# Performance work log

Hardware: AMD Instinct MI355X
Metric: run time of the kernel (lower is better)

Reference implementation:

```python
import jax, jax.numpy as jnp
import numpy as np

B, N_IN, N_MID, N_OUT = 262144, 64, 128, 32


def setup_inputs() -> dict:
    key = jax.random.key(0)
    kx, k1, kb1, k2, kb2 = jax.random.split(key, 5)
    v1 = 1.0 / np.sqrt(N_IN)   # per-synapse init range sqrt(1/len(dendrites))
    v2 = 1.0 / np.sqrt(N_MID)
    return {
        "x": jax.random.normal(kx, (B, N_IN), dtype=jnp.float32),
        "W1": jax.random.uniform(k1, (N_IN, N_MID), minval=-v1, maxval=v1, dtype=jnp.float32),
        "b1": jnp.zeros((N_MID,), dtype=jnp.float32),  # obtain_float_parameter inits biases to 0.0
        "W2": jax.random.uniform(k2, (N_MID, N_OUT), minval=-v2, maxval=v2, dtype=jnp.float32),
        "b2": jnp.zeros((N_OUT,), dtype=jnp.float32),
    }


def reference(x, W1, b1, W2, b2):
    # RegularNeuron: sum_i k_ij * x_i + b_j, then ReLU
    h = jax.nn.relu(x @ W1 + b1)          # [B, N_MID]
    # Output DestinationNeuron: sum_j k_jo * h_j + b_o, no activation
    y = h @ W2 + b2                        # [B, N_OUT]
    return y
```

## Files before the change

### kernel.cpp

```cpp
#include <hip/hip_runtime.h>
#include <hip/hip_bf16.h>

#define B_ROWS 262144
#define N_TILES (B_ROWS / 16)

typedef short short8 __attribute__((ext_vector_type(8)));
typedef float f32x4 __attribute__((ext_vector_type(4)));

__device__ inline short f2bf(float f) {
    __hip_bfloat16 h = __float2bfloat16(f);
    return __builtin_bit_cast(short, h);
}
__device__ inline unsigned pk2(float a, float b) {
    unsigned lo = (unsigned short)f2bf(a);
    unsigned hi = (unsigned short)f2bf(b);
    return lo | (hi << 16);
}

__global__ __launch_bounds__(256, 2) void livenet_mlp(
    const float* __restrict__ x, const float* __restrict__ W1,
    const float* __restrict__ b1, const float* __restrict__ W2,
    const float* __restrict__ b2, float* __restrict__ y) {
    __shared__ __align__(16) short hbuf[4 * 2048];

    const int tid  = threadIdx.x;
    const int wid  = tid >> 6;
    const int lane = tid & 63;
    const int g    = lane >> 4;
    const int q    = lane & 15;
    short* hb = hbuf + wid * 2048;
    const int key = 2 * (q & 7);

    short8 w1f[2][8];
#pragma unroll
    for (int ks = 0; ks < 2; ++ks)
#pragma unroll
        for (int n = 0; n < 8; ++n) {
            short8 v;
#pragma unroll
            for (int j = 0; j < 8; ++j)
                v[j] = f2bf(W1[(ks * 32 + g * 8 + j) * 128 + n * 16 + q]);
            w1f[ks][n] = v;
        }
    short8 w2f[4][2];
#pragma unroll
    for (int ks = 0; ks < 4; ++ks)
#pragma unroll
        for (int n = 0; n < 2; ++n) {
            short8 v;
#pragma unroll
            for (int j = 0; j < 8; ++j)
                v[j] = f2bf(W2[(ks * 32 + g * 8 + j) * 32 + n * 16 + q]);
            w2f[ks][n] = v;
        }
    f32x4 binit1[8], binit2[2];
#pragma unroll
    for (int n = 0; n < 8; ++n)
        binit1[n] = *(const f32x4*)(b1 + n * 16 + 4 * g);
#pragma unroll
    for (int n = 0; n < 2; ++n)
        binit2[n] = *(const f32x4*)(b2 + n * 16 + 4 * g);

    const int gwave = blockIdx.x * 4 + wid;
    const int S     = gridDim.x * 4;

    const float* xl = x + (size_t)q * 64 + g * 8;

    f32x4 c0, c1, c2, c3, m0, m1, m2, m3;
    {
        const f32x4* p = (const f32x4*)(xl + (size_t)gwave * 1024);
        c0 = p[0]; c1 = p[1]; c2 = p[8]; c3 = p[9];
    }
    {
        const f32x4* p = (const f32x4*)(xl + (size_t)(gwave + S) * 1024);
        m0 = p[0]; m1 = p[1]; m2 = p[8]; m3 = p[9];
    }

    for (int tile = gwave; tile < N_TILES; tile += S) {
        const int t2 = (tile + 2 * S < N_TILES) ? (tile + 2 * S) : tile;
        f32x4 p0, p1, p2, p3;
        {
            const f32x4* p = (const f32x4*)(xl + (size_t)t2 * 1024);
            p0 = p[0]; p1 = p[1]; p2 = p[8]; p3 = p[9];
        }

        const int row0 = tile * 16;

        short8 a0, a1;
        {
            short8 v;
            v[0] = f2bf(c0[0]); v[1] = f2bf(c0[1]); v[2] = f2bf(c0[2]); v[3] = f2bf(c0[3]);
            v[4] = f2bf(c1[0]); v[5] = f2bf(c1[1]); v[6] = f2bf(c1[2]); v[7] = f2bf(c1[3]);
            a0 = v;
            v[0] = f2bf(c2[0]); v[1] = f2bf(c2[1]); v[2] = f2bf(c2[2]); v[3] = f2bf(c2[3]);
            v[4] = f2bf(c3[0]); v[5] = f2bf(c3[1]); v[6] = f2bf(c3[2]); v[7] = f2bf(c3[3]);
            a1 = v;
        }

        f32x4 acc1[8];
#pragma unroll
        for (int n = 0; n < 8; ++n) {
            acc1[n] = __builtin_amdgcn_mfma_f32_16x16x32_bf16(w1f[0][n], a0, binit1[n], 0, 0, 0);
            acc1[n] = __builtin_amdgcn_mfma_f32_16x16x32_bf16(w1f[1][n], a1, acc1[n], 0, 0, 0);
        }

#pragma unroll
        for (int n = 0; n < 8; ++n) {
            float h0 = fmaxf(acc1[n][0], 0.0f);
            float h1 = fmaxf(acc1[n][1], 0.0f);
            float h2 = fmaxf(acc1[n][2], 0.0f);
            float h3 = fmaxf(acc1[n][3], 0.0f);
            uint2 w;
            w.x = pk2(h0, h1);
            w.y = pk2(h2, h3);
            const int cbp = (4 * n + g) ^ key;
            ((uint2*)hb)[q * 32 + cbp] = w;
        }

        short8 ha[4];
#pragma unroll
        for (int ks = 0; ks < 4; ++ks) {
            const int cbr = (8 * ks + 2 * g) ^ key;
            ha[ks] = *(const short8*)&hb[q * 128 + 4 * cbr];
        }

        f32x4 acc2[2];
#pragma unroll
        for (int n = 0; n < 2; ++n) {
            acc2[n] = __builtin_amdgcn_mfma_f32_16x16x32_bf16(w2f[0][n], ha[0], binit2[n], 0, 0, 0);
#pragma unroll
            for (int ks = 1; ks < 4; ++ks)
                acc2[n] = __builtin_amdgcn_mfma_f32_16x16x32_bf16(w2f[ks][n], ha[ks], acc2[n], 0, 0, 0);
        }

#pragma unroll
        for (int n = 0; n < 2; ++n)
            __builtin_nontemporal_store(
                acc2[n], (f32x4*)(y + (size_t)(row0 + q) * 32 + n * 16 + 4 * g));

        c0 = m0; c1 = m1; c2 = m2; c3 = m3;
        m0 = p0; m1 = p1; m2 = p2; m3 = p3;
    }
}

extern "C" void kernel_launch(void* const* d_in, const int* in_sizes, int n_in,
                              void* d_out, int out_size, void* d_ws, size_t ws_size,
                              hipStream_t stream) {
    const float* x  = (const float*)d_in[0];
    const float* W1 = (const float*)d_in[1];
    const float* b1 = (const float*)d_in[2];
    const float* W2 = (const float*)d_in[3];
    const float* b2 = (const float*)d_in[4];
    float* y = (float*)d_out;

    const int blocks = 512;
    livenet_mlp<<<blocks, 256, 0, stream>>>(x, W1, b1, W2, b2, y);
}
```

Baseline: 24.80 us.

## Stage weights through LDS with coalesced loads, shorten prefetch depth, plain stores

```diff
diff --git a/kernel.cpp b/kernel.cpp
--- a/kernel.cpp
+++ b/kernel.cpp
@@ -22,6 +22,9 @@
     const float* __restrict__ b1, const float* __restrict__ W2,
     const float* __restrict__ b2, float* __restrict__ y) {
     __shared__ __align__(16) short hbuf[4 * 2048];
+    __shared__ __align__(16) short w1t[128 * 64];
+    __shared__ __align__(16) short w2t[32 * 128];
+    __shared__ __align__(16) float bls[160];
 
     const int tid  = threadIdx.x;
     const int wid  = tid >> 6;
@@ -31,57 +34,60 @@
     short* hb = hbuf + wid * 2048;
     const int key = 2 * (q & 7);
 
+#pragma unroll
+    for (int p = 0; p < 8; ++p) {
+        const int idx = p * 1024 + tid * 4;
+        f32x4 v = *(const f32x4*)(W1 + idx);
+        const int k = idx >> 7, c = idx & 127;
+#pragma unroll
+        for (int e = 0; e < 4; ++e) w1t[(c + e) * 64 + k] = f2bf(v[e]);
+    }
+#pragma unroll
+    for (int p = 0; p < 4; ++p) {
+        const int idx = p * 1024 + tid * 4;
+        f32x4 v = *(const f32x4*)(W2 + idx);
+        const int k = idx >> 5, o = idx & 31;
+#pragma unroll
+        for (int e = 0; e < 4; ++e) w2t[(o + e) * 128 + k] = f2bf(v[e]);
+    }
+    if (tid < 128) bls[tid] = b1[tid];
+    else if (tid < 160) bls[tid] = b2[tid - 128];
+    __syncthreads();
+
     short8 w1f[2][8];
 #pragma unroll
     for (int ks = 0; ks < 2; ++ks)
 #pragma unroll
-        for (int n = 0; n < 8; ++n) {
-            short8 v;
-#pragma unroll
-            for (int j = 0; j < 8; ++j)
-                v[j] = f2bf(W1[(ks * 32 + g * 8 + j) * 128 + n * 16 + q]);
-            w1f[ks][n] = v;
-        }
+        for (int n = 0; n < 8; ++n)
+            w1f[ks][n] = *(const short8*)&w1t[(n * 16 + q) * 64 + ks * 32 + g * 8];
     short8 w2f[4][2];
 #pragma unroll
     for (int ks = 0; ks < 4; ++ks)
 #pragma unroll
-        for (int n = 0; n < 2; ++n) {
-            short8 v;
-#pragma unroll
-            for (int j = 0; j < 8; ++j)
-                v[j] = f2bf(W2[(ks * 32 + g * 8 + j) * 32 + n * 16 + q]);
-            w2f[ks][n] = v;
-        }
+        for (int n = 0; n < 2; ++n)
+            w2f[ks][n] = *(const short8*)&w2t[(n * 16 + q) * 128 + ks * 32 + g * 8];
     f32x4 binit1[8], binit2[2];
 #pragma unroll
-    for (int n = 0; n < 8; ++n)
-        binit1[n] = *(const f32x4*)(b1 + n * 16 + 4 * g);
+    for (int n = 0; n < 8; ++n) binit1[n] = *(const f32x4*)&bls[n * 16 + 4 * g];
 #pragma unroll
-    for (int n = 0; n < 2; ++n)
-        binit2[n] = *(const f32x4*)(b2 + n * 16 + 4 * g);
+    for (int n = 0; n < 2; ++n) binit2[n] = *(const f32x4*)&bls[128 + n * 16 + 4 * g];
 
     const int gwave = blockIdx.x * 4 + wid;
     const int S     = gridDim.x * 4;
-
     const float* xl = x + (size_t)q * 64 + g * 8;
 
-    f32x4 c0, c1, c2, c3, m0, m1, m2, m3;
+    f32x4 c0, c1, c2, c3;
     {
         const f32x4* p = (const f32x4*)(xl + (size_t)gwave * 1024);
         c0 = p[0]; c1 = p[1]; c2 = p[8]; c3 = p[9];
     }
-    {
-        const f32x4* p = (const f32x4*)(xl + (size_t)(gwave + S) * 1024);
-        m0 = p[0]; m1 = p[1]; m2 = p[8]; m3 = p[9];
-    }
 
     for (int tile = gwave; tile < N_TILES; tile += S) {
-        const int t2 = (tile + 2 * S < N_TILES) ? (tile + 2 * S) : tile;
+        const int tn = (tile + S < N_TILES) ? (tile + S) : tile;
         f32x4 p0, p1, p2, p3;
         {
-            const f32x4* p = (const f32x4*)(xl + (size_t)t2 * 1024);
-            p0 = p[0]; p1 = p[1]; p2 = p[8]; p3 = p[9];
+            const f32x4* pp = (const f32x4*)(xl + (size_t)tn * 1024);
+            p0 = pp[0]; p1 = pp[1]; p2 = pp[8]; p3 = pp[9];
         }
 
         const int row0 = tile * 16;
@@ -135,11 +141,9 @@
 
 #pragma unroll
         for (int n = 0; n < 2; ++n)
-            __builtin_nontemporal_store(
-                acc2[n], (f32x4*)(y + (size_t)(row0 + q) * 32 + n * 16 + 4 * g));
+            *(f32x4*)(y + (size_t)(row0 + q) * 32 + n * 16 + 4 * g) = acc2[n];
 
-        c0 = m0; c1 = m1; c2 = m2; c3 = m3;
-        m0 = p0; m1 = p1; m2 = p2; m3 = p3;
+        c0 = p0; c1 = p1; c2 = p2; c3 = p3;
     }
 }
 
```

New measurement: 28.46 us. 14.8% more time.

## Move W2 and biases to LDS, shorten prefetch, raise occupancy to 3 blocks/CU

Applied to the files above, without the earlier changes.

```diff
diff --git a/kernel.cpp b/kernel.cpp
--- a/kernel.cpp
+++ b/kernel.cpp
@@ -6,6 +6,7 @@
 
 typedef short short8 __attribute__((ext_vector_type(8)));
 typedef float f32x4 __attribute__((ext_vector_type(4)));
+struct U2x2 { uint2 a, b; };
 
 __device__ inline short f2bf(float f) {
     __hip_bfloat16 h = __float2bfloat16(f);
@@ -17,19 +18,30 @@
     return lo | (hi << 16);
 }
 
-__global__ __launch_bounds__(256, 2) void livenet_mlp(
+__global__ __launch_bounds__(256, 3) void livenet_mlp(
     const float* __restrict__ x, const float* __restrict__ W1,
     const float* __restrict__ b1, const float* __restrict__ W2,
     const float* __restrict__ b2, float* __restrict__ y) {
-    __shared__ __align__(16) short hbuf[4 * 2048];
+    __shared__ __align__(16) uint2 hbu[4 * 512];
+    __shared__ __align__(16) short w2t[32 * 136];
+    __shared__ __align__(16) float bls[160];
 
     const int tid  = threadIdx.x;
     const int wid  = tid >> 6;
     const int lane = tid & 63;
     const int g    = lane >> 4;
     const int q    = lane & 15;
-    short* hb = hbuf + wid * 2048;
+    uint2* hb = hbu + wid * 512;
     const int key = 2 * (q & 7);
+
+#pragma unroll
+    for (int p = 0; p < 16; ++p) {
+        const int idx = p * 256 + tid;
+        w2t[(idx & 31) * 136 + (idx >> 5)] = f2bf(W2[idx]);
+    }
+    if (tid < 128) bls[tid] = b1[tid];
+    else if (tid < 160) bls[tid] = b2[tid - 128];
+    __syncthreads();
 
     short8 w1f[2][8];
 #pragma unroll
@@ -42,46 +54,25 @@
                 v[j] = f2bf(W1[(ks * 32 + g * 8 + j) * 128 + n * 16 + q]);
             w1f[ks][n] = v;
         }
-    short8 w2f[4][2];
-#pragma unroll
-    for (int ks = 0; ks < 4; ++ks)
-#pragma unroll
-        for (int n = 0; n < 2; ++n) {
-            short8 v;
-#pragma unroll
-            for (int j = 0; j < 8; ++j)
-                v[j] = f2bf(W2[(ks * 32 + g * 8 + j) * 32 + n * 16 + q]);
-            w2f[ks][n] = v;
-        }
-    f32x4 binit1[8], binit2[2];
-#pragma unroll
-    for (int n = 0; n < 8; ++n)
-        binit1[n] = *(const f32x4*)(b1 + n * 16 + 4 * g);
-#pragma unroll
-    for (int n = 0; n < 2; ++n)
-        binit2[n] = *(const f32x4*)(b2 + n * 16 + 4 * g);
 
     const int gwave = blockIdx.x * 4 + wid;
     const int S     = gridDim.x * 4;
-
     const float* xl = x + (size_t)q * 64 + g * 8;
 
-    f32x4 c0, c1, c2, c3, m0, m1, m2, m3;
+    const volatile f32x4*  bv  = (const volatile f32x4*)bls;
+    #define W2V(nr, off) (*(const volatile short8*)&w2t[(nr) * 136 + (off)])
+
+    f32x4 cur0, cur1, cur2, cur3, nxt0, nxt1, nxt2, nxt3;
     {
         const f32x4* p = (const f32x4*)(xl + (size_t)gwave * 1024);
-        c0 = p[0]; c1 = p[1]; c2 = p[8]; c3 = p[9];
-    }
-    {
-        const f32x4* p = (const f32x4*)(xl + (size_t)(gwave + S) * 1024);
-        m0 = p[0]; m1 = p[1]; m2 = p[8]; m3 = p[9];
+        cur0 = p[0]; cur1 = p[1]; cur2 = p[8]; cur3 = p[9];
     }
 
     for (int tile = gwave; tile < N_TILES; tile += S) {
-        const int t2 = (tile + 2 * S < N_TILES) ? (tile + 2 * S) : tile;
-        f32x4 p0, p1, p2, p3;
-        {
-            const f32x4* p = (const f32x4*)(xl + (size_t)t2 * 1024);
-            p0 = p[0]; p1 = p[1]; p2 = p[8]; p3 = p[9];
+        const int tn = tile + S;
+        if (tn < N_TILES) {
+            const f32x4* p = (const f32x4*)(xl + (size_t)tn * 1024);
+            nxt0 = p[0]; nxt1 = p[1]; nxt2 = p[8]; nxt3 = p[9];
         }
 
         const int row0 = tile * 16;
@@ -89,48 +80,47 @@
         short8 a0, a1;
         {
             short8 v;
-            v[0] = f2bf(c0[0]); v[1] = f2bf(c0[1]); v[2] = f2bf(c0[2]); v[3] = f2bf(c0[3]);
-            v[4] = f2bf(c1[0]); v[5] = f2bf(c1[1]); v[6] = f2bf(c1[2]); v[7] = f2bf(c1[3]);
+            v[0] = f2bf(cur0[0]); v[1] = f2bf(cur0[1]); v[2] = f2bf(cur0[2]); v[3] = f2bf(cur0[3]);
+            v[4] = f2bf(cur1[0]); v[5] = f2bf(cur1[1]); v[6] = f2bf(cur1[2]); v[7] = f2bf(cur1[3]);
             a0 = v;
-            v[0] = f2bf(c2[0]); v[1] = f2bf(c2[1]); v[2] = f2bf(c2[2]); v[3] = f2bf(c2[3]);
-            v[4] = f2bf(c3[0]); v[5] = f2bf(c3[1]); v[6] = f2bf(c3[2]); v[7] = f2bf(c3[3]);
+            v[0] = f2bf(cur2[0]); v[1] = f2bf(cur2[1]); v[2] = f2bf(cur2[2]); v[3] = f2bf(cur2[3]);
+            v[4] = f2bf(cur3[0]); v[5] = f2bf(cur3[1]); v[6] = f2bf(cur3[2]); v[7] = f2bf(cur3[3]);
             a1 = v;
         }
 
         f32x4 acc1[8];
 #pragma unroll
         for (int n = 0; n < 8; ++n) {
-            acc1[n] = __builtin_amdgcn_mfma_f32_16x16x32_bf16(w1f[0][n], a0, binit1[n], 0, 0, 0);
+            acc1[n] = bv[n * 4 + g];
+            acc1[n] = __builtin_amdgcn_mfma_f32_16x16x32_bf16(w1f[0][n], a0, acc1[n], 0, 0, 0);
             acc1[n] = __builtin_amdgcn_mfma_f32_16x16x32_bf16(w1f[1][n], a1, acc1[n], 0, 0, 0);
         }
 
 #pragma unroll
         for (int n = 0; n < 8; ++n) {
-            float h0 = fmaxf(acc1[n][0], 0.0f);
-            float h1 = fmaxf(acc1[n][1], 0.0f);
-            float h2 = fmaxf(acc1[n][2], 0.0f);
-            float h3 = fmaxf(acc1[n][3], 0.0f);
             uint2 w;
-            w.x = pk2(h0, h1);
-            w.y = pk2(h2, h3);
-            const int cbp = (4 * n + g) ^ key;
-            ((uint2*)hb)[q * 32 + cbp] = w;
+            w.x = pk2(fmaxf(acc1[n][0], 0.0f), fmaxf(acc1[n][1], 0.0f));
+            w.y = pk2(fmaxf(acc1[n][2], 0.0f), fmaxf(acc1[n][3], 0.0f));
+            hb[q * 32 + ((4 * n + g) ^ key)] = w;
         }
 
         short8 ha[4];
 #pragma unroll
         for (int ks = 0; ks < 4; ++ks) {
-            const int cbr = (8 * ks + 2 * g) ^ key;
-            ha[ks] = *(const short8*)&hb[q * 128 + 4 * cbr];
+            const int jj = q * 32 + ((8 * ks + 2 * g) ^ key);
+            U2x2 t{hb[jj], hb[jj + 1]};
+            ha[ks] = __builtin_bit_cast(short8, t);
         }
 
         f32x4 acc2[2];
 #pragma unroll
         for (int n = 0; n < 2; ++n) {
-            acc2[n] = __builtin_amdgcn_mfma_f32_16x16x32_bf16(w2f[0][n], ha[0], binit2[n], 0, 0, 0);
+            acc2[n] = bv[32 + n * 4 + g];
 #pragma unroll
-            for (int ks = 1; ks < 4; ++ks)
-                acc2[n] = __builtin_amdgcn_mfma_f32_16x16x32_bf16(w2f[ks][n], ha[ks], acc2[n], 0, 0, 0);
+            for (int ks = 0; ks < 4; ++ks) {
+                short8 w = W2V(n * 16 + q, ks * 32 + g * 8);
+                acc2[n] = __builtin_amdgcn_mfma_f32_16x16x32_bf16(w, ha[ks], acc2[n], 0, 0, 0);
+            }
         }
 
 #pragma unroll
@@ -138,9 +128,9 @@
             __builtin_nontemporal_store(
                 acc2[n], (f32x4*)(y + (size_t)(row0 + q) * 32 + n * 16 + 4 * g));
 
-        c0 = m0; c1 = m1; c2 = m2; c3 = m3;
-        m0 = p0; m1 = p1; m2 = p2; m3 = p3;
+        cur0 = nxt0; cur1 = nxt1; cur2 = nxt2; cur3 = nxt3;
     }
+    #undef W2V
 }
 
 extern "C" void kernel_launch(void* const* d_in, const int* in_sizes, int n_in,
@@ -153,6 +143,6 @@
     const float* b2 = (const float*)d_in[4];
     float* y = (float*)d_out;
 
-    const int blocks = 512;
+    const int blocks = 768;
     livenet_mlp<<<blocks, 256, 0, stream>>>(x, W1, b1, W2, b2, y);
 }
```

Measured after the change: 34.03 us. 1.37x slower.

## Permute hidden-layer columns so MFMA outputs feed second GEMM directly from registers

Applied to the files above, without the earlier changes.

```diff
diff --git a/kernel.cpp b/kernel.cpp
--- a/kernel.cpp
+++ b/kernel.cpp
@@ -11,35 +11,27 @@
     __hip_bfloat16 h = __float2bfloat16(f);
     return __builtin_bit_cast(short, h);
 }
-__device__ inline unsigned pk2(float a, float b) {
-    unsigned lo = (unsigned short)f2bf(a);
-    unsigned hi = (unsigned short)f2bf(b);
-    return lo | (hi << 16);
-}
 
 __global__ __launch_bounds__(256, 2) void livenet_mlp(
     const float* __restrict__ x, const float* __restrict__ W1,
     const float* __restrict__ b1, const float* __restrict__ W2,
     const float* __restrict__ b2, float* __restrict__ y) {
-    __shared__ __align__(16) short hbuf[4 * 2048];
-
     const int tid  = threadIdx.x;
     const int wid  = tid >> 6;
     const int lane = tid & 63;
     const int g    = lane >> 4;
     const int q    = lane & 15;
-    short* hb = hbuf + wid * 2048;
-    const int key = 2 * (q & 7);
 
     short8 w1f[2][8];
 #pragma unroll
     for (int ks = 0; ks < 2; ++ks)
 #pragma unroll
         for (int n = 0; n < 8; ++n) {
+            const int pc = 32 * (n & 3) + 8 * (q >> 2) + 4 * (n >> 2) + (q & 3);
             short8 v;
 #pragma unroll
             for (int j = 0; j < 8; ++j)
-                v[j] = f2bf(W1[(ks * 32 + g * 8 + j) * 128 + n * 16 + q]);
+                v[j] = f2bf(W1[(ks * 32 + g * 8 + j) * 128 + pc]);
             w1f[ks][n] = v;
         }
     short8 w2f[4][2];
@@ -56,32 +48,26 @@
     f32x4 binit1[8], binit2[2];
 #pragma unroll
     for (int n = 0; n < 8; ++n)
-        binit1[n] = *(const f32x4*)(b1 + n * 16 + 4 * g);
+        binit1[n] = *(const f32x4*)(b1 + 32 * (n & 3) + 8 * g + 4 * (n >> 2));
 #pragma unroll
     for (int n = 0; n < 2; ++n)
         binit2[n] = *(const f32x4*)(b2 + n * 16 + 4 * g);
 
     const int gwave = blockIdx.x * 4 + wid;
     const int S     = gridDim.x * 4;
-
     const float* xl = x + (size_t)q * 64 + g * 8;
 
-    f32x4 c0, c1, c2, c3, m0, m1, m2, m3;
+    f32x4 cur0, cur1, cur2, cur3, nxt0, nxt1, nxt2, nxt3;
     {
         const f32x4* p = (const f32x4*)(xl + (size_t)gwave * 1024);
-        c0 = p[0]; c1 = p[1]; c2 = p[8]; c3 = p[9];
-    }
-    {
-        const f32x4* p = (const f32x4*)(xl + (size_t)(gwave + S) * 1024);
-        m0 = p[0]; m1 = p[1]; m2 = p[8]; m3 = p[9];
+        cur0 = p[0]; cur1 = p[1]; cur2 = p[8]; cur3 = p[9];
     }
 
     for (int tile = gwave; tile < N_TILES; tile += S) {
-        const int t2 = (tile + 2 * S < N_TILES) ? (tile + 2 * S) : tile;
-        f32x4 p0, p1, p2, p3;
-        {
-            const f32x4* p = (const f32x4*)(xl + (size_t)t2 * 1024);
-            p0 = p[0]; p1 = p[1]; p2 = p[8]; p3 = p[9];
+        const int tn = tile + S;
+        if (tn < N_TILES) {
+            const f32x4* p = (const f32x4*)(xl + (size_t)tn * 1024);
+            nxt0 = p[0]; nxt1 = p[1]; nxt2 = p[8]; nxt3 = p[9];
         }
 
         const int row0 = tile * 16;
@@ -89,11 +75,11 @@
         short8 a0, a1;
         {
             short8 v;
-            v[0] = f2bf(c0[0]); v[1] = f2bf(c0[1]); v[2] = f2bf(c0[2]); v[3] = f2bf(c0[3]);
-            v[4] = f2bf(c1[0]); v[5] = f2bf(c1[1]); v[6] = f2bf(c1[2]); v[7] = f2bf(c1[3]);
+            v[0] = f2bf(cur0[0]); v[1] = f2bf(cur0[1]); v[2] = f2bf(cur0[2]); v[3] = f2bf(cur0[3]);
+            v[4] = f2bf(cur1[0]); v[5] = f2bf(cur1[1]); v[6] = f2bf(cur1[2]); v[7] = f2bf(cur1[3]);
             a0 = v;
-            v[0] = f2bf(c2[0]); v[1] = f2bf(c2[1]); v[2] = f2bf(c2[2]); v[3] = f2bf(c2[3]);
-            v[4] = f2bf(c3[0]); v[5] = f2bf(c3[1]); v[6] = f2bf(c3[2]); v[7] = f2bf(c3[3]);
+            v[0] = f2bf(cur2[0]); v[1] = f2bf(cur2[1]); v[2] = f2bf(cur2[2]); v[3] = f2bf(cur2[3]);
+            v[4] = f2bf(cur3[0]); v[5] = f2bf(cur3[1]); v[6] = f2bf(cur3[2]); v[7] = f2bf(cur3[3]);
             a1 = v;
         }
 
@@ -104,24 +90,19 @@
             acc1[n] = __builtin_amdgcn_mfma_f32_16x16x32_bf16(w1f[1][n], a1, acc1[n], 0, 0, 0);
         }
 
-#pragma unroll
-        for (int n = 0; n < 8; ++n) {
-            float h0 = fmaxf(acc1[n][0], 0.0f);
-            float h1 = fmaxf(acc1[n][1], 0.0f);
-            float h2 = fmaxf(acc1[n][2], 0.0f);
-            float h3 = fmaxf(acc1[n][3], 0.0f);
-            uint2 w;
-            w.x = pk2(h0, h1);
-            w.y = pk2(h2, h3);
-            const int cbp = (4 * n + g) ^ key;
-            ((uint2*)hb)[q * 32 + cbp] = w;
-        }
-
         short8 ha[4];
 #pragma unroll
         for (int ks = 0; ks < 4; ++ks) {
-            const int cbr = (8 * ks + 2 * g) ^ key;
-            ha[ks] = *(const short8*)&hb[q * 128 + 4 * cbr];
+            short8 v;
+            v[0] = f2bf(fmaxf(acc1[ks][0], 0.0f));
+            v[1] = f2bf(fmaxf(acc1[ks][1], 0.0f));
+            v[2] = f2bf(fmaxf(acc1[ks][2], 0.0f));
+            v[3] = f2bf(fmaxf(acc1[ks][3], 0.0f));
+            v[4] = f2bf(fmaxf(acc1[ks + 4][0], 0.0f));
+            v[5] = f2bf(fmaxf(acc1[ks + 4][1], 0.0f));
+            v[6] = f2bf(fmaxf(acc1[ks + 4][2], 0.0f));
+            v[7] = f2bf(fmaxf(acc1[ks + 4][3], 0.0f));
+            ha[ks] = v;
         }
 
         f32x4 acc2[2];
@@ -138,8 +119,7 @@
             __builtin_nontemporal_store(
                 acc2[n], (f32x4*)(y + (size_t)(row0 + q) * 32 + n * 16 + 4 * g));
 
-        c0 = m0; c1 = m1; c2 = m2; c3 = m3;
-        m0 = p0; m1 = p1; m2 = p2; m3 = p3;
+        cur0 = nxt0; cur1 = nxt1; cur2 = nxt2; cur3 = nxt3;
     }
 }
 
```

New measurement: 24.47 us. No clear change (-1.3%).
